# Performance work log

Hardware: AMD Instinct MI355X
Metric: run time of the kernel (lower is better)

Reference implementation:

```python
import jax, jax.numpy as jnp
import numpy as np

B, T, DIM, MC = 64, 128, 768, 30  # batch, seq len, input_dim, middle_channel


def _cdist(a, b):
    # torch.cdist(a, b, p=2): [B,T,d] x [B,T,d] -> [B,T,T]
    sq = (jnp.sum(a * a, -1)[:, :, None] + jnp.sum(b * b, -1)[:, None, :]
          - 2.0 * jnp.einsum('bid,bjd->bij', a, b))
    return jnp.sqrt(jnp.clip(sq, 1e-12))


def _conv(x, w, b):
    # NCHW 'same' conv, stride 1
    y = jax.lax.conv_general_dilated(x, w, (1, 1), 'SAME',
                                     dimension_numbers=('NCHW', 'OIHW', 'NCHW'))
    return y + b[None, :, None, None]


def setup_inputs() -> dict:
    key = jax.random.key(0)
    ks = jax.random.split(key, 10)
    q_seq = jax.random.normal(ks[0], (B, T, DIM), jnp.float32)
    k_seq = jax.random.normal(ks[1], (B, T, DIM), jnp.float32)
    q_len_seq = jax.random.randint(ks[2], (B, 1), 1, T + 1).astype(jnp.int32)
    k_len_seq = jax.random.randint(ks[3], (B, 1), 1, T + 1).astype(jnp.int32)
    q_R = jax.random.uniform(ks[4], (B, T), jnp.float32)
    k_R = jax.random.uniform(ks[5], (B, T), jnp.float32)
    conv1_w = jax.random.normal(ks[6], (MC, 2, 5, 5), jnp.float32) * 0.05
    conv2_w = jax.random.normal(ks[7], (MC, MC, 5, 5), jnp.float32) * 0.02
    conv3_w = jax.random.normal(ks[8], (1, MC, 3, 3), jnp.float32) * 0.05
    conv1_b = jnp.zeros((MC,), jnp.float32)
    conv2_b = jnp.zeros((MC,), jnp.float32)
    conv3_b = jnp.zeros((1,), jnp.float32)
    return dict(q_seq=q_seq, q_len_seq=q_len_seq, q_R=q_R,
                k_seq=k_seq, k_len_seq=k_len_seq, k_R=k_R,
                conv1_w=conv1_w, conv1_b=conv1_b,
                conv2_w=conv2_w, conv2_b=conv2_b,
                conv3_w=conv3_w, conv3_b=conv3_b)


def reference(q_seq, q_len_seq, q_R, k_seq, k_len_seq, k_R,
              conv1_w, conv1_b, conv2_w, conv2_b, conv3_w, conv3_b):
    bsz = q_seq.shape[0]
    Tq = q_seq.shape[1]
    D = _cdist(q_seq, k_seq)                                  # [B,T,T]
    P = jnp.abs(q_R[:, :, None] - k_R[:, None, :])            # cdist on 1-d R
    pos = jnp.arange(Tq, dtype=jnp.int32)
    row_mask = pos[None, :] < q_len_seq                       # [B,T]
    col_mask = pos[None, :] < k_len_seq                       # [B,T]
    mask = row_mask[:, :, None] & col_mask[:, None, :]        # [B,T,T]
    maskf = mask.astype(D.dtype)
    D = D * maskf
    P = P * maskf
    A = jnp.stack([D, P], axis=1)                             # [B,2,T,T]
    A = jax.nn.relu(_conv(A, conv1_w, conv1_b))
    A = jax.nn.relu(_conv(A, conv2_w, conv2_b))
    A = _conv(A, conv3_w, conv3_b)[:, 0] + D                  # [B,T,T]
    A = jnp.where(mask, A, jnp.float32(100.0))
    A = jax.nn.softmax(-A, axis=2)
    At = A.reshape(bsz, Tq * Tq)
    At = At / jnp.sum(jnp.abs(At), axis=1, keepdims=True)     # L1 normalize
    dis = jnp.einsum('bn,bn->b', D.reshape(bsz, Tq * Tq), At)
    return (A, dis)
```

## Files before the change

### kernel.cpp

```cpp
#include <hip/hip_runtime.h>
#include <hip/hip_bf16.h>
#include <stdint.h>

using u16 = unsigned short;
using u32 = unsigned int;
using u8  = unsigned char;

#define NB 64
#define TT 128
#define DK 768
#define MC 30

typedef float f32x16 __attribute__((ext_vector_type(16)));
typedef __bf16 bf16x8 __attribute__((ext_vector_type(8)));
typedef long long ll;
typedef __attribute__((ext_vector_type(2))) ll ll2;
#if __has_builtin(__builtin_amdgcn_mfma_scale_f32_32x32x64_f8f6f4)
#define HAVE_MXFP8 1
typedef int i32x8 __attribute__((ext_vector_type(8)));
#endif
#if __has_builtin(__builtin_amdgcn_global_load_lds)
#define HAVE_GLDS 1
#endif

__device__ inline void unpack2(u32 u, float& lo, float& hi){
  union{u32 i; float f;} a, b; a.i = u << 16; b.i = u & 0xFFFF0000u; lo = a.f; hi = b.f;
}
__device__ inline u16 f2bf(float f){
  union{u32 i; float f;} v; v.f = f;
  u32 r = v.i + 0x7FFFu + ((v.i >> 16) & 1u);
  return (u16)(r >> 16);
}
__device__ inline u32 pack2bf(float a, float b){ return (u32)f2bf(a) | ((u32)f2bf(b) << 16); }

#if __has_builtin(__builtin_amdgcn_cvt_pk_fp8_f32)
template<bool HIW>
__device__ inline u32 pk_fp8(float a, float b, u32 old){
  return (u32)__builtin_amdgcn_cvt_pk_fp8_f32(a, b, (int)old, HIW);
}
#else
__device__ inline u8 f2fp8_1(float f){
  union{float f; u32 u;} v; v.f = f;
  u32 s = (v.u >> 24) & 0x80u;
  u32 abs = v.u & 0x7fffffffu;
  if (abs < 0x3c800000u){
    float sc = fabsf(f) * 512.0f;
    int m = (int)rintf(sc);
    return (u8)(s | (u32)m);
  }
  u32 e8 = abs >> 23; u32 mant = abs & 0x7fffffu;
  u32 m3 = mant >> 20; u32 rest = mant & 0xfffffu;
  u32 rb = (rest > 0x80000u) || (rest == 0x80000u && (m3 & 1u));
  m3 += rb;
  u32 E = e8 - 120u;
  if (m3 == 8u){ m3 = 0u; E += 1u; }
  if (E >= 16u || (E == 15u && m3 == 7u)) return (u8)(s | 0x7Eu);
  return (u8)(s | (E << 3) | m3);
}
template<bool HIW>
__device__ inline u32 pk_fp8(float a, float b, u32 old){
  u32 w = (u32)f2fp8_1(a) | ((u32)f2fp8_1(b) << 8);
  return HIW ? ((old & 0x0000FFFFu) | (w << 16)) : ((old & 0xFFFF0000u) | w);
}
#endif

#if __has_builtin(__builtin_amdgcn_cvt_pk_f32_fp8)
__device__ inline void upk_fp8x4(u32 w, float* x){
  auto a0 = __builtin_amdgcn_cvt_pk_f32_fp8((int)w, false);
  auto a1 = __builtin_amdgcn_cvt_pk_f32_fp8((int)w, true);
  x[0] = a0[0]; x[1] = a0[1]; x[2] = a1[0]; x[3] = a1[1];
}
#else
__device__ inline float fp8_1(u32 byte){
  u32 s = (byte & 0x80u) << 24;
  u32 E = (byte >> 3) & 15u, M = byte & 7u;
  union{u32 u; float f;} v;
  if (E == 0){ v.f = (float)M * (1.0f/512.0f); v.u |= s; }
  else v.u = s | ((E + 120u) << 23) | (M << 20);
  return v.f;
}
__device__ inline void upk_fp8x4(u32 w, float* x){
  x[0] = fp8_1(w & 255u); x[1] = fp8_1((w >> 8) & 255u);
  x[2] = fp8_1((w >> 16) & 255u); x[3] = fp8_1(w >> 24);
}
#endif

__global__ __launch_bounds__(256) void prep_w_k(const float* __restrict__ w2,
    const float* __restrict__ w1, u8* __restrict__ w2p, u16* __restrict__ w1c){
  int bidx = blockIdx.x;
  if (bidx < 25){
    int tap = bidx;
    int i = threadIdx.x;
    int oc = i >> 3, q = i & 7, ic0 = q * 4;
    float v[4];
    #pragma unroll
    for (int j = 0; j < 4; ++j)
      v[j] = (oc < MC && ic0 + j < MC) ? w2[(oc*MC + ic0 + j)*25 + tap] : 0.f;
    u32 w = pk_fp8<false>(v[0], v[1], 0u);
    w = pk_fp8<true>(v[2], v[3], w);
    int lo = ((oc << 5) + (q << 2)) ^ ((oc & 7) << 4);
    *(u32*)(w2p + tap*1024 + lo) = w;
  } else {
    for (int i = threadIdx.x; i < 2560; i += 256){
      int dy = i >> 9; int rem = i & 511; int oc = rem >> 4; int k = rem & 15;
      int dx = k >> 1, c = k & 1;
      float v = (oc < MC && dx < 5) ? w1[(oc*2 + c)*25 + dy*5 + dx] : 0.f;
      int byteoff = dy*1024 + (((oc<<5) + (k<<1)) ^ ((oc&7)<<4));
      *(u16*)((char*)w1c + byteoff) = f2bf(v);
    }
  }
}

__global__ __launch_bounds__(256) void row_norms_k(const float* __restrict__ q, const float* __restrict__ k,
    float* __restrict__ qq, float* __restrict__ kk,
    u16* __restrict__ qb16, u16* __restrict__ kb16){
  int wave = blockIdx.x * 4 + (threadIdx.x >> 6);
  int lane = threadIdx.x & 63;
  const float* src; float* dst; u16* bdst; int row;
  if (wave < NB * TT) { src = q; dst = qq; bdst = qb16; row = wave; }
  else                { src = k; dst = kk; bdst = kb16; row = wave - NB * TT; }
  const float4* p = (const float4*)(src + (size_t)row * DK);
  char* ob = (char*)(bdst + (size_t)row * DK);
  int key = (row & 7) << 4;
  float s = 0.f;
  {
    float4 a = p[2*lane], b2 = p[2*lane + 1];
    s += a.x*a.x + a.y*a.y + a.z*a.z + a.w*a.w;
    s += b2.x*b2.x + b2.y*b2.y + b2.z*b2.z + b2.w*b2.w;
    uint4 st;
    st.x = pack2bf(a.x, a.y);  st.y = pack2bf(a.z, a.w);
    st.z = pack2bf(b2.x, b2.y); st.w = pack2bf(b2.z, b2.w);
    *(uint4*)(ob + ((lane << 4) ^ key)) = st;
  }
  if (lane < 32){
    int g = 64 + lane;
    float4 a = p[2*g], b2 = p[2*g + 1];
    s += a.x*a.x + a.y*a.y + a.z*a.z + a.w*a.w;
    s += b2.x*b2.x + b2.y*b2.y + b2.z*b2.z + b2.w*b2.w;
    uint4 st;
    st.x = pack2bf(a.x, a.y);  st.y = pack2bf(a.z, a.w);
    st.z = pack2bf(b2.x, b2.y); st.w = pack2bf(b2.z, b2.w);
    *(uint4*)(ob + ((g << 4) ^ key)) = st;
  }
  #pragma unroll
  for (int o = 32; o; o >>= 1) s += __shfl_xor(s, o);
  if (lane == 0) dst[row] = s;
}

__global__ __launch_bounds__(256) void cdist_mfma_k(
    const u16* __restrict__ Qb16, const u16* __restrict__ Kb16,
    const float* __restrict__ qq, const float* __restrict__ kk,
    const int* __restrict__ qlen, const int* __restrict__ klen,
    const float* __restrict__ qR, const float* __restrict__ kR,
    float* __restrict__ Dout, u32* __restrict__ inb){
  __shared__ __align__(16) char qs[32 * 1536];
  __shared__ __align__(16) char ksm[128 * 256];
  int rt = blockIdx.x;
  int b  = blockIdx.y;
  int r0 = rt * 32;
  int tid = threadIdx.x;
  int lane = tid & 63, w = tid >> 6;
  int hi = lane >> 5, l31 = lane & 31;
  const char* Qg = (const char*)(Qb16 + ((size_t)b * TT + r0) * DK);
  const char* Kg = (const char*)(Kb16 + (size_t)b * TT * DK);
#ifdef HAVE_GLDS
  #pragma unroll
  for (int i = 0; i < 12; ++i){
    int gb = (i*4 + w) << 6;
    __builtin_amdgcn_global_load_lds((const u32*)(Qg + ((gb + lane) << 4)),
                                     (u32*)(qs + (gb << 4)), 16, 0, 0);
  }
#else
  for (int idx = tid; idx < 3072; idx += 256)
    *(uint4*)(qs + idx*16) = *(const uint4*)(Qg + idx*16);
#endif
  int col = w * 32 + l31;
  f32x16 acc;
  #pragma unroll
  for (int r = 0; r < 16; ++r) acc[r] = 0.f;
  for (int kc = 0; kc < DK; kc += 128){
    __syncthreads();
#ifdef HAVE_GLDS
    const char* Ks = Kg + kc*2;
    #pragma unroll
    for (int i = 0; i < 8; ++i){
      int gb = (i*4 + w) << 6;
      int g = gb + lane;
      __builtin_amdgcn_global_load_lds((const u32*)(Ks + (g >> 4)*1536 + ((g & 15) << 4)),
                                       (u32*)(ksm + (gb << 4)), 16, 0, 0);
    }
#else
    for (int idx = tid; idx < 2048; idx += 256){
      int c = idx >> 4, j = idx & 15;
      *(uint4*)(ksm + idx*16) = *(const uint4*)(Kg + c*1536 + kc*2 + j*16);
    }
#endif
    __syncthreads();
    #pragma unroll
    for (int k8 = 0; k8 < 8; ++k8){
      bf16x8 a  = *(const bf16x8*)(qs  + l31 * 1536 + (((kc + k8*16 + hi*8) * 2) ^ ((l31 & 7) << 4)));
      bf16x8 bv = *(const bf16x8*)(ksm + col * 256  + (((k8*16 + hi*8) * 2) ^ ((col & 7) << 4)));
      acc = __builtin_amdgcn_mfma_f32_32x32x16_bf16(a, bv, acc, 0, 0, 0);
    }
  }
  int ql = qlen[b], kl = klen[b];
  float kkv = kk[b * TT + col];
  float krv = kR[b * TT + col];
  bool cm = col < kl;
  #pragma unroll
  for (int r = 0; r < 16; ++r){
    int row = r0 + (r & 3) + 8 * (r >> 2) + 4 * hi;
    float qqv = qq[b * TT + row];
    float sq = qqv + kkv - 2.f * acc[r];
    float d = sqrtf(fmaxf(sq, 1e-12f));
    bool m = (row < ql) && cm;
    float dm = m ? d : 0.f;
    float pm = m ? fabsf(qR[b * TT + row] - krv) : 0.f;
    Dout[(((size_t)b * TT + row) << 7) + col] = dm;
    inb[(((size_t)b * TT + row) << 7) + col] = pack2bf(dm, pm);
  }
}

#define C1_ROWW 136
#define C2_IN_ROWB 4224
#define F_INB_BYTES (16*C1_ROWW*4)
#define F_C2_OFF F_INB_BYTES
#define F_SMEM (F_INB_BYTES + 12*C2_IN_ROWB)

__global__ __launch_bounds__(512, 4) void conv12_mfma_k(
    const u32* __restrict__ inb, const u8* __restrict__ w2p, const u16* __restrict__ w1c,
    const float* __restrict__ b1, const float* __restrict__ b2, u8* __restrict__ act2){
  __shared__ __align__(16) char smem[F_SMEM];
  u32* ilds = (u32*)smem;
  char* c2in = smem + F_C2_OFF;
  int o  = blockIdx.x;
  int yg = ((o & 7) << 1) + (o >> 3);
  int bb = blockIdx.y;
  int y0 = yg * 8;
  int tid = threadIdx.x;
  for (int i = tid; i < 16*C1_ROWW; i += 512){
    int r = i / C1_ROWW, xi = i - r * C1_ROWW;
    int gy = y0 - 4 + r, gx = xi - 2;
    u32 v = 0;
    if ((unsigned)gy < 128u && (unsigned)gx < 128u)
      v = inb[(((size_t)bb * 128 + gy) << 7) + gx];
    ilds[r * C1_ROWW + xi] = v;
  }
  for (int i = tid; i < 96; i += 512){
    int r = i >> 3; int rem = i & 7; int ci = rem >> 1; int h = rem & 1;
    int lx = (ci < 2) ? ci : (128 + ci);
    int addr = r*C2_IN_ROWB + (((lx << 5) + (h << 4)) ^ ((lx & 7) << 4));
    *(uint4*)(c2in + addr) = make_uint4(0,0,0,0);
  }
  int lane = tid & 63, w = tid >> 6;
  int hi = lane >> 5, l31 = lane & 31;
  int aSwz = ((l31 << 5) + (hi << 4)) ^ ((l31 & 7) << 4);
  bf16x8 afr[5];
  #pragma unroll
  for (int dy = 0; dy < 5; ++dy)
    afr[dy] = *(const bf16x8*)((const char*)w1c + dy*1024 + aSwz);
  float b1v[16];
  #pragma unroll
  for (int r = 0; r < 16; ++r){
    int oc = (r & 3) + 8*(r >> 2) + 4*hi;
    b1v[r] = (oc < MC) ? b1[oc] : 0.f;
  }
  __syncthreads();
  for (int rep = 0; rep < 2; ++rep){
    if (rep == 1 && w >= 4) break;
    int idx = (rep == 0) ? w : (8 + w);
    int gy = y0 - 2 + idx;
    bool oob = (unsigned)gy >= 128u;
    #pragma unroll
    for (int t = 0; t < 4; ++t){
      int px = t*32 + l31;
      u32 words[4];
      if (!oob){
        f32x16 acc;
        #pragma unroll
        for (int r = 0; r < 16; ++r) acc[r] = 0.f;
        #pragma unroll
        for (int dy = 0; dy < 5; ++dy){
          const u32* rp = &ilds[(idx + dy)*C1_ROWW + px + hi*4];
          union { u32 uw[4]; bf16x8 v; } ub;
          ub.uw[0] = rp[0]; ub.uw[1] = rp[1]; ub.uw[2] = rp[2]; ub.uw[3] = rp[3];
          acc = __builtin_amdgcn_mfma_f32_32x32x16_bf16(afr[dy], ub.v, acc, 0, 0, 0);
        }
        #pragma unroll
        for (int q = 0; q < 4; ++q){
          u32 word = pk_fp8<false>(fmaxf(acc[4*q+0]+b1v[4*q+0], 0.f),
                                   fmaxf(acc[4*q+1]+b1v[4*q+1], 0.f), 0u);
          word = pk_fp8<true>(fmaxf(acc[4*q+2]+b1v[4*q+2], 0.f),
                              fmaxf(acc[4*q+3]+b1v[4*q+3], 0.f), word);
          words[q] = word;
        }
      } else {
        words[0] = words[1] = words[2] = words[3] = 0u;
      }
      int lx = px + 2;
      #pragma unroll
      for (int q = 0; q < 4; ++q){
        int ic = q*8 + hi*4;
        int addr = idx*C2_IN_ROWB + (((lx << 5) + ic) ^ ((lx & 7) << 4));
        *(u32*)(c2in + addr) = words[q];
      }
    }
  }
  __syncthreads();
  f32x16 acc[4];
  #pragma unroll
  for (int t = 0; t < 4; ++t)
    #pragma unroll
    for (int r = 0; r < 16; ++r) acc[t][r] = 0.f;
  #pragma unroll
  for (int dy = 0; dy < 5; ++dy){
    const char* rowp = c2in + (w + dy)*C2_IN_ROWB;
    ll2 aw[5];
    #pragma unroll
    for (int dx = 0; dx < 5; ++dx)
      aw[dx] = *(const ll2*)(w2p + (dy*5 + dx)*1024 + aSwz);
#ifdef HAVE_MXFP8
    union U8x { struct { ll2 lo, hi; } p; i32x8 v; };
    U8x a01, a23, a4z;
    ll2 zz; zz.x = 0; zz.y = 0;
    a01.p.lo = aw[0]; a01.p.hi = aw[1];
    a23.p.lo = aw[2]; a23.p.hi = aw[3];
    a4z.p.lo = aw[4]; a4z.p.hi = zz;
    #pragma unroll
    for (int t = 0; t < 4; ++t){
      int pxb = t*32 + l31;
      ll2 bl[5];
      #pragma unroll
      for (int dx = 0; dx < 5; ++dx){
        int px2 = pxb + dx;
        int boff = ((px2 << 5) + (hi << 4)) ^ ((px2 & 7) << 4);
        bl[dx] = *(const ll2*)(rowp + boff);
      }
      U8x b01, b23, b4d;
      b01.p.lo = bl[0]; b01.p.hi = bl[1];
      b23.p.lo = bl[2]; b23.p.hi = bl[3];
      b4d.p.lo = bl[4]; b4d.p.hi = bl[4];
      acc[t] = __builtin_amdgcn_mfma_scale_f32_32x32x64_f8f6f4(
                 a01.v, b01.v, acc[t], 0, 0, 0, 0x7F7F7F7F, 0, 0x7F7F7F7F);
      acc[t] = __builtin_amdgcn_mfma_scale_f32_32x32x64_f8f6f4(
                 a23.v, b23.v, acc[t], 0, 0, 0, 0x7F7F7F7F, 0, 0x7F7F7F7F);
      acc[t] = __builtin_amdgcn_mfma_scale_f32_32x32x64_f8f6f4(
                 a4z.v, b4d.v, acc[t], 0, 0, 0, 0x7F7F7F7F, 0, 0x7F7F7F7F);
    }
#else
    #pragma unroll
    for (int dx = 0; dx < 5; ++dx){
      ll2 a = aw[dx];
      #pragma unroll
      for (int t = 0; t < 4; ++t){
        int px2 = t*32 + l31 + dx;
        int boff = ((px2 << 5) + (hi << 4)) ^ ((px2 & 7) << 4);
        ll2 b = *(const ll2*)(rowp + boff);
        acc[t] = __builtin_amdgcn_mfma_f32_32x32x16_fp8_fp8(a.x, b.x, acc[t], 0, 0, 0);
        acc[t] = __builtin_amdgcn_mfma_f32_32x32x16_fp8_fp8(a.y, b.y, acc[t], 0, 0, 0);
      }
    }
#endif
  }
  float b2v[16];
  #pragma unroll
  for (int r = 0; r < 16; ++r){
    int oc = (r & 3) + 8*(r >> 2) + 4*hi;
    b2v[r] = (oc < MC) ? b2[oc] : 0.f;
  }
  __syncthreads();
  int wbase = w * 4096;
  #pragma unroll
  for (int t = 0; t < 4; ++t){
    int px = t*32 + l31;
    #pragma unroll
    for (int q = 0; q < 4; ++q){
      float v0 = fmaxf(acc[t][4*q+0] + b2v[4*q+0], 0.f);
      float v1 = fmaxf(acc[t][4*q+1] + b2v[4*q+1], 0.f);
      float v2 = fmaxf(acc[t][4*q+2] + b2v[4*q+2], 0.f);
      float v3 = fmaxf(acc[t][4*q+3] + b2v[4*q+3], 0.f);
      u32 word = pk_fp8<false>(v0, v1, 0u);
      word = pk_fp8<true>(v2, v3, word);
      int addr = wbase + (((px<<5) + (q<<3) + (hi<<2)) ^ (((px>>2)&3)<<3));
      *(u32*)(c2in + addr) = word;
    }
  }
  int y = y0 + w;
  #pragma unroll
  for (int p = 0; p < 8; ++p){
    int x = p*16 + (lane >> 2), cg = lane & 3;
    int addr = wbase + (((x<<5) + (cg<<3)) ^ (((x>>2)&3)<<3));
    uint2 v = *(const uint2*)(c2in + addr);
    *(uint2*)(act2 + ((((size_t)bb*128 + y)*128 + x) << 5) + cg*8) = v;
  }
}

__global__ __launch_bounds__(512) void conv3sm_k(const u8* __restrict__ act2,
    const float* __restrict__ w3, const float* __restrict__ b3, const float* __restrict__ Dbuf,
    const int* __restrict__ qlen, const int* __restrict__ klen,
    float* __restrict__ Aout, float* __restrict__ rowsum, int b0){
  __shared__ float wlds[9][32];
  __shared__ float ex0[512], ex2[512];
  __shared__ float redm[8], reds[8], redd[8];
  int o  = blockIdx.x;
  int i  = ((o & 7) << 4) + (o >> 3);
  int bb = blockIdx.y;
  int b  = b0 + bb;
  int tid = threadIdx.x;
  for (int idx = tid; idx < 288; idx += 512){
    int tap = idx >> 5, c = idx & 31;
    wlds[tap][c] = (c < MC) ? w3[c * 9 + tap] : 0.f;
  }
  __syncthreads();
  int px = tid >> 2, cg = tid & 3, wv = tid >> 6;
  float T0 = 0.f, T1 = 0.f, T2 = 0.f;
  #pragma unroll
  for (int dy = 0; dy < 3; ++dy){
    int gy = i - 1 + dy;
    uint2 v = make_uint2(0, 0);
    if ((unsigned)gy < 128u)
      v = *(const uint2*)(act2 + ((((size_t)bb*128 + gy)*128 + px) << 5) + cg*8);
    float x[8];
    upk_fp8x4(v.x, x);
    upk_fp8x4(v.y, x + 4);
    const float* w0p = &wlds[dy*3 + 0][cg*8];
    const float* w1p = &wlds[dy*3 + 1][cg*8];
    const float* w2q = &wlds[dy*3 + 2][cg*8];
    #pragma unroll
    for (int c = 0; c < 8; ++c){
      T0 = fmaf(x[c], w0p[c], T0);
      T1 = fmaf(x[c], w1p[c], T1);
      T2 = fmaf(x[c], w2q[c], T2);
    }
  }
  ex0[tid] = T0; ex2[tid] = T2;
  __syncthreads();
  float acc = T1;
  if (px > 0)   acc += ex0[tid - 4];
  if (px < 127) acc += ex2[tid + 4];
  acc += __shfl_xor(acc, 1);
  acc += __shfl_xor(acc, 2);
  acc += b3[0];
  float Dv = Dbuf[(((size_t)b * 128 + i) << 7) + px];
  bool m = (i < qlen[b]) && (px < klen[b]);
  float xv = m ? -(acc + Dv) : -100.f;
  float mx = xv;
  #pragma unroll
  for (int o2 = 32; o2; o2 >>= 1) mx = fmaxf(mx, __shfl_xor(mx, o2));
  if ((tid & 63) == 0) redm[wv] = mx;
  __syncthreads();
  mx = fmaxf(fmaxf(fmaxf(redm[0], redm[1]), fmaxf(redm[2], redm[3])),
             fmaxf(fmaxf(redm[4], redm[5]), fmaxf(redm[6], redm[7])));
  float e = __expf(xv - mx);
  float s  = e;
  float de = Dv * e;
  #pragma unroll
  for (int o2 = 32; o2; o2 >>= 1){ s += __shfl_xor(s, o2); de += __shfl_xor(de, o2); }
  if ((tid & 63) == 0){ reds[wv] = s; redd[wv] = de; }
  __syncthreads();
  float s8  = (reds[0] + reds[1]) + (reds[2] + reds[3]) + (reds[4] + reds[5]) + (reds[6] + reds[7]);
  float a = e * 4.0f / s8;
  if (cg == 0) Aout[(((size_t)b * 128 + i) << 7) + px] = a;
  if (tid == 0){
    float d8 = (redd[0] + redd[1]) + (redd[2] + redd[3]) + (redd[4] + redd[5]) + (redd[6] + redd[7]);
    rowsum[b * TT + i] = d8 / s8;
  }
}

__global__ __launch_bounds__(128) void dis_k(const float* __restrict__ rowsum, float* __restrict__ out){
  int b = blockIdx.x, tid = threadIdx.x;
  float v = rowsum[b * TT + tid];
  #pragma unroll
  for (int o = 32; o; o >>= 1) v += __shfl_xor(v, o);
  __shared__ float red[2];
  if ((tid & 63) == 0) red[tid >> 6] = v;
  __syncthreads();
  if (tid == 0) out[b] = (red[0] + red[1]) * (1.0f / 128.0f);
}

extern "C" void kernel_launch(void* const* d_in, const int* in_sizes, int n_in,
                              void* d_out, int out_size, void* d_ws, size_t ws_size,
                              hipStream_t stream){
  const float* q_seq = (const float*)d_in[0];
  const int*   q_len = (const int*)d_in[1];
  const float* q_R   = (const float*)d_in[2];
  const float* k_seq = (const float*)d_in[3];
  const int*   k_len = (const int*)d_in[4];
  const float* k_R   = (const float*)d_in[5];
  const float* c1w   = (const float*)d_in[6];
  const float* c1b   = (const float*)d_in[7];
  const float* c2w   = (const float*)d_in[8];
  const float* c2b   = (const float*)d_in[9];
  const float* c3w   = (const float*)d_in[10];
  const float* c3b   = (const float*)d_in[11];
  float* out = (float*)d_out;

  char* base = (char*)d_ws;
  size_t off = 0;
  auto take = [&](size_t bytes)->char*{
    char* p = base + off;
    off = (off + bytes + 255) & ~(size_t)255;
    return p;
  };
  float* Dbuf   = (float*)take((size_t)NB * TT * TT * 4);
  float* qq     = (float*)take((size_t)NB * TT * 4);
  float* kkn    = (float*)take((size_t)NB * TT * 4);
  float* rowsum = (float*)take((size_t)NB * TT * 4);
  u32*   inb    = (u32*)  take((size_t)NB * TT * TT * 4);
  u8*    w2p    = (u8*)   take(25 * 1024);
  u16*   w1c    = (u16*)  take(5 * 1024);
  u16*   qb16   = (u16*)  take((size_t)NB * TT * DK * 2);
  u16*   kb16   = (u16*)  take((size_t)NB * TT * DK * 2);
  size_t fixed = off;
  int BCH = 64;
  while (BCH > 1 && fixed + (size_t)BCH * TT * TT * 32 + 1024 > ws_size) BCH >>= 1;
  u8* act2 = (u8*)take((size_t)BCH * TT * TT * 32);

  prep_w_k<<<26, 256, 0, stream>>>(c2w, c1w, w2p, w1c);
  row_norms_k<<<4096, 256, 0, stream>>>(q_seq, k_seq, qq, kkn, qb16, kb16);
  cdist_mfma_k<<<dim3(4, NB), 256, 0, stream>>>(qb16, kb16, qq, kkn, q_len, k_len, q_R, k_R, Dbuf, inb);
  for (int b0 = 0; b0 < NB; b0 += BCH){
    int nb = BCH;
    conv12_mfma_k<<<dim3(16, nb), 512, 0, stream>>>(inb + (size_t)b0 * TT * TT, w2p, w1c, c1b, c2b, act2);
    conv3sm_k<<<dim3(TT, nb), 512, 0, stream>>>(act2, c3w, c3b, Dbuf, q_len, k_len, out, rowsum, b0);
  }
  dis_k<<<NB, 128, 0, stream>>>(rowsum, out + (size_t)NB * TT * TT);
}
```

Before: 104.5 us.

## Process two rows per conv3 block and swizzle cdist block-to-XCD mapping

The conv3+softmax kernel now has each 512-thread block handle two output rows, with each thread loading 16 fp8 channels instead of 8. This halves the grid and removes one shuffle stage, and the softmax reductions are split per row across 4 waves. Separately, the cdist kernel switches to a 1-D grid with a swizzled mapping of block index to (batch, row tile), likely to spread batches across XCDs for better L2 locality of the K tiles. The trade is fewer, wider blocks with more registers per thread.

```diff
diff --git a/kernel.cpp b/kernel.cpp
--- a/kernel.cpp
+++ b/kernel.cpp
@@ -155,8 +155,9 @@
     float* __restrict__ Dout, u32* __restrict__ inb){
   __shared__ __align__(16) char qs[32 * 1536];
   __shared__ __align__(16) char ksm[128 * 256];
-  int rt = blockIdx.x;
-  int b  = blockIdx.y;
+  int bid = blockIdx.x;
+  int b  = ((bid & 7) << 3) + (bid >> 5);
+  int rt = (bid >> 3) & 3;
   int r0 = rt * 32;
   int tid = threadIdx.x;
   int lane = tid & 63, w = tid >> 6;
@@ -403,7 +404,7 @@
   __shared__ float ex0[512], ex2[512];
   __shared__ float redm[8], reds[8], redd[8];
   int o  = blockIdx.x;
-  int i  = ((o & 7) << 4) + (o >> 3);
+  int ip = ((o & 7) << 3) + (o >> 3);
   int bb = blockIdx.y;
   int b  = b0 + bb;
   int tid = threadIdx.x;
@@ -412,22 +413,26 @@
     wlds[tap][c] = (c < MC) ? w3[c * 9 + tap] : 0.f;
   }
   __syncthreads();
-  int px = tid >> 2, cg = tid & 3, wv = tid >> 6;
+  int r  = tid >> 8;
+  int t  = tid & 255;
+  int px = t >> 1, half = t & 1;
+  int i  = ip * 2 + r;
+  int wv = tid >> 6;
   float T0 = 0.f, T1 = 0.f, T2 = 0.f;
   #pragma unroll
   for (int dy = 0; dy < 3; ++dy){
     int gy = i - 1 + dy;
-    uint2 v = make_uint2(0, 0);
+    uint4 v = make_uint4(0, 0, 0, 0);
     if ((unsigned)gy < 128u)
-      v = *(const uint2*)(act2 + ((((size_t)bb*128 + gy)*128 + px) << 5) + cg*8);
-    float x[8];
-    upk_fp8x4(v.x, x);
-    upk_fp8x4(v.y, x + 4);
-    const float* w0p = &wlds[dy*3 + 0][cg*8];
-    const float* w1p = &wlds[dy*3 + 1][cg*8];
-    const float* w2q = &wlds[dy*3 + 2][cg*8];
-    #pragma unroll
-    for (int c = 0; c < 8; ++c){
+      v = *(const uint4*)(act2 + ((((size_t)bb*128 + gy)*128 + px) << 5) + half*16);
+    float x[16];
+    upk_fp8x4(v.x, x); upk_fp8x4(v.y, x + 4);
+    upk_fp8x4(v.z, x + 8); upk_fp8x4(v.w, x + 12);
+    const float* w0p = &wlds[dy*3 + 0][half*16];
+    const float* w1p = &wlds[dy*3 + 1][half*16];
+    const float* w2q = &wlds[dy*3 + 2][half*16];
+    #pragma unroll
+    for (int c = 0; c < 16; ++c){
       T0 = fmaf(x[c], w0p[c], T0);
       T1 = fmaf(x[c], w1p[c], T1);
       T2 = fmaf(x[c], w2q[c], T2);
@@ -436,10 +441,9 @@
   ex0[tid] = T0; ex2[tid] = T2;
   __syncthreads();
   float acc = T1;
-  if (px > 0)   acc += ex0[tid - 4];
-  if (px < 127) acc += ex2[tid + 4];
+  if (px > 0)   acc += ex0[tid - 2];
+  if (px < 127) acc += ex2[tid + 2];
   acc += __shfl_xor(acc, 1);
-  acc += __shfl_xor(acc, 2);
   acc += b3[0];
   float Dv = Dbuf[(((size_t)b * 128 + i) << 7) + px];
   bool m = (i < qlen[b]) && (px < klen[b]);
@@ -449,8 +453,8 @@
   for (int o2 = 32; o2; o2 >>= 1) mx = fmaxf(mx, __shfl_xor(mx, o2));
   if ((tid & 63) == 0) redm[wv] = mx;
   __syncthreads();
-  mx = fmaxf(fmaxf(fmaxf(redm[0], redm[1]), fmaxf(redm[2], redm[3])),
-             fmaxf(fmaxf(redm[4], redm[5]), fmaxf(redm[6], redm[7])));
+  int rb4 = r << 2;
+  mx = fmaxf(fmaxf(redm[rb4], redm[rb4+1]), fmaxf(redm[rb4+2], redm[rb4+3]));
   float e = __expf(xv - mx);
   float s  = e;
   float de = Dv * e;
@@ -458,12 +462,12 @@
   for (int o2 = 32; o2; o2 >>= 1){ s += __shfl_xor(s, o2); de += __shfl_xor(de, o2); }
   if ((tid & 63) == 0){ reds[wv] = s; redd[wv] = de; }
   __syncthreads();
-  float s8  = (reds[0] + reds[1]) + (reds[2] + reds[3]) + (reds[4] + reds[5]) + (reds[6] + reds[7]);
-  float a = e * 4.0f / s8;
-  if (cg == 0) Aout[(((size_t)b * 128 + i) << 7) + px] = a;
-  if (tid == 0){
-    float d8 = (redd[0] + redd[1]) + (redd[2] + redd[3]) + (redd[4] + redd[5]) + (redd[6] + redd[7]);
-    rowsum[b * TT + i] = d8 / s8;
+  float s4 = (reds[rb4] + reds[rb4+1]) + (reds[rb4+2] + reds[rb4+3]);
+  float a = e * 2.0f / s4;
+  if (half == 0) Aout[(((size_t)b * 128 + i) << 7) + px] = a;
+  if (t == 0){
+    float d4 = (redd[rb4] + redd[rb4+1]) + (redd[rb4+2] + redd[rb4+3]);
+    rowsum[b * TT + i] = d4 / s4;
   }
 }
 
@@ -518,11 +522,11 @@
 
   prep_w_k<<<26, 256, 0, stream>>>(c2w, c1w, w2p, w1c);
   row_norms_k<<<4096, 256, 0, stream>>>(q_seq, k_seq, qq, kkn, qb16, kb16);
-  cdist_mfma_k<<<dim3(4, NB), 256, 0, stream>>>(qb16, kb16, qq, kkn, q_len, k_len, q_R, k_R, Dbuf, inb);
+  cdist_mfma_k<<<256, 256, 0, stream>>>(qb16, kb16, qq, kkn, q_len, k_len, q_R, k_R, Dbuf, inb);
   for (int b0 = 0; b0 < NB; b0 += BCH){
     int nb = BCH;
     conv12_mfma_k<<<dim3(16, nb), 512, 0, stream>>>(inb + (size_t)b0 * TT * TT, w2p, w1c, c1b, c2b, act2);
-    conv3sm_k<<<dim3(TT, nb), 512, 0, stream>>>(act2, c3w, c3b, Dbuf, q_len, k_len, out, rowsum, b0);
+    conv3sm_k<<<dim3(64, nb), 512, 0, stream>>>(act2, c3w, c3b, Dbuf, q_len, k_len, out, rowsum, b0);
   }
   dis_k<<<NB, 128, 0, stream>>>(rowsum, out + (size_t)NB * TT * TT);
 }
```

New measurement: 98.53 us. 1.06x faster.
